# Kernel optimization log

Measured on AMD Instinct MI355X. Metric: run time of the kernel, lower is better.

## Reference

```python
import jax, jax.numpy as jnp
import numpy as np

B = 16384          # batch size
NUM_NEG = 4
N = 1 + NUM_NEG    # items per row (pos + negs)
D = 128            # embedding_dim
F = 4              # num_factors
FS = D // F        # factor_size = 32
TD = 384           # bert_text_dim
NU = 100000        # num_users
NI = 100000        # num_items
HID = 150          # text MLP hidden
M = 2              # num_modalities


def _linear_init(k, fan_out, fan_in):
    bound = 1.0 / np.sqrt(fan_in)
    return jax.random.uniform(k, (fan_out, fan_in), jnp.float32, -bound, bound)


def setup_inputs() -> dict:
    key = jax.random.key(0)
    ks = jax.random.split(key, 12)
    batch = jax.random.randint(ks[0], (B, 1 + N), 0, NU)          # col0=user, cols1..5=items
    text = jax.random.normal(ks[1], (B, N, TD), dtype=jnp.float32)
    user_table = jax.random.normal(ks[2], (NU, D), dtype=jnp.float32)
    item_table = jax.random.normal(ks[3], (NI, D), dtype=jnp.float32)
    w1 = _linear_init(ks[4], HID, TD)
    b1 = jax.random.uniform(ks[5], (HID,), jnp.float32, -1/np.sqrt(TD), 1/np.sqrt(TD))
    w2 = _linear_init(ks[6], D, HID)
    b2 = jax.random.uniform(ks[7], (D,), jnp.float32, -1/np.sqrt(HID), 1/np.sqrt(HID))
    # per-factor attention MLPs, stacked over the F factors (all same size here)
    aw1 = jax.random.uniform(ks[8], (F, M, 3 * FS), jnp.float32, -1/np.sqrt(3*FS), 1/np.sqrt(3*FS))
    ab1 = jax.random.uniform(ks[9], (F, M), jnp.float32, -1/np.sqrt(3*FS), 1/np.sqrt(3*FS))
    aw2 = jax.random.uniform(ks[10], (F, M, M), jnp.float32, -1/np.sqrt(M), 1/np.sqrt(M))
    return dict(batch=batch, text=text, user_table=user_table, item_table=item_table,
                w1=w1, b1=b1, w2=w2, b2=b2, aw1=aw1, ab1=ab1, aw2=aw2)


def _leaky_relu(x):
    return jnp.where(x > 0, x, 0.01 * x)


def reference(batch, text, user_table, item_table, w1, b1, w2, b2, aw1, ab1, aw2):
    # text MLP: Linear -> LeakyReLU -> Linear -> LeakyReLU
    te = _leaky_relu(_leaky_relu(text @ w1.T + b1) @ w2.T + b2)   # [B,N,D]

    users = batch[:, 0]
    items = batch[:, 1:]
    u = user_table[users]                                          # [B,D]
    ie = item_table[items]                                         # [B,N,D]

    # split into F factors of size FS (vectorized over factor dim)
    uf = jnp.broadcast_to(u[:, None, :], ie.shape).reshape(B, N, F, FS)
    itf = ie.reshape(B, N, F, FS)
    tf = te.reshape(B, N, F, FS)

    cat = jnp.concatenate([uf, itf, tf], axis=-1)                  # [B,N,F,3*FS]
    nrm = jnp.linalg.norm(cat, axis=-1, keepdims=True)
    cat = cat / jnp.maximum(nrm, 1e-12)                            # F.normalize(dim=-1)

    h = jnp.tanh(jnp.einsum('bnfk,fmk->bnfm', cat, aw1) + ab1)     # [B,N,F,M]
    logits = jnp.einsum('bnfm,fom->bnfo', h, aw2)                  # [B,N,F,M]
    # torch nn.Softmax() with dim=None on a 3D tensor -> softmax over dim 0 (batch)
    attn = jax.nn.softmax(logits, axis=0)

    r_ui = attn[..., 0] * jax.nn.softplus(jnp.sum(uf * itf, axis=-1))  # [B,N,F]
    r_ut = attn[..., 1] * jax.nn.softplus(jnp.sum(uf * tf, axis=-1))   # [B,N,F]
    ratings = jnp.sum(r_ui + r_ut, axis=-1)                        # [B,N], sum over factors
    return ratings
```

## Files before the change

kernel.cpp:

```cpp
#include <hip/hip_runtime.h>
#include <hip/hip_bf16.h>

#define TDIM 384
#define HID 150
#define DD 128
#define ROWS 81920
#define RT 64

typedef __attribute__((ext_vector_type(8))) short short8;
typedef __attribute__((ext_vector_type(4))) float f32x4;

#define SMEM_BYTES 35840

__device__ __forceinline__ float lrelu(float x) { return x > 0.f ? x : 0.01f * x; }
__device__ __forceinline__ float softplusf(float x) {
    return fmaxf(x, 0.f) + log1pf(expf(-fabsf(x)));
}

__device__ __forceinline__ short8 pack8(const float4 a, const float4 b) {
    union { short8 s; __hip_bfloat16 h[8]; } u;
    u.h[0] = __float2bfloat16(a.x); u.h[1] = __float2bfloat16(a.y);
    u.h[2] = __float2bfloat16(a.z); u.h[3] = __float2bfloat16(a.w);
    u.h[4] = __float2bfloat16(b.x); u.h[5] = __float2bfloat16(b.y);
    u.h[6] = __float2bfloat16(b.z); u.h[7] = __float2bfloat16(b.w);
    return u.s;
}

__global__ __launch_bounds__(256)
void prep_w(const float* __restrict__ w1, const float* __restrict__ w2,
            short8* __restrict__ w1f, short8* __restrict__ w2f)
{
    const int idx = blockIdx.x * 256 + threadIdx.x;
    union { short8 s; __hip_bfloat16 h[8]; } u;
    if (idx < 7680) {
        const int kt = idx / 640, c = idx % 640;
        const int col = c >> 2, q = c & 3;
        const int k = kt * 32 + q * 8;
#pragma unroll
        for (int j = 0; j < 8; ++j)
            u.h[j] = __float2bfloat16(col < HID ? w1[(size_t)col * TDIM + k + j] : 0.f);
        w1f[idx] = u.s;
    } else if (idx < 10240) {
        const int i2 = idx - 7680;
        const int kt = i2 / 512, c = i2 % 512;
        const int col = c >> 2, q = c & 3;
        const int k = kt * 32 + q * 8;
#pragma unroll
        for (int j = 0; j < 8; ++j)
            u.h[j] = __float2bfloat16((k + j) < HID ? w2[(size_t)col * HID + k + j] : 0.f);
        w2f[i2] = u.s;
    }
}

__global__ __launch_bounds__(256, 4)
void fused_main(const int* __restrict__ batch,
                const float* __restrict__ text,
                const float* __restrict__ user_table,
                const float* __restrict__ item_table,
                const short8* __restrict__ w1f,
                const float* __restrict__ b1,
                const short8* __restrict__ w2f,
                const float* __restrict__ b2,
                const float* __restrict__ aw1,
                const float* __restrict__ ab1,
                const float* __restrict__ aw2,
                float* __restrict__ expp,
                float* __restrict__ Sglob)
{
    __shared__ __align__(16) unsigned char smem[SMEM_BYTES];
    __shared__ float S_lds[40];
    __hip_bfloat16* Hs = (__hip_bfloat16*)(smem);
    float*          Ts = (float*)(smem);

    const int t    = threadIdx.x;
    const int r0   = blockIdx.x * RT;
    const int lane = t & 63;
    const int wv   = t >> 6;
    const int m16  = lane & 15;
    const int quad = lane >> 4;
    const int wr   = (wv & 1) * 32;
    const int wc   = (wv >> 1) * 80;
    const int wc2  = (wv >> 1) * 64;

    const int srow = t >> 2;
    const int sko  = (t & 3) * 8;
    const bool hasx = (t < 128);

    const int p3row = t >> 2;
    const int p3f   = t & 3;
    const int gr    = r0 + p3row;
    const int bb    = gr / 5;
    const int nn    = gr - bb * 5;
    const int uid   = batch[bb * 6];
    const int iid   = batch[bb * 6 + 1 + nn];

    if (t < 40) S_lds[t] = 0.f;

    f32x4 acc1[2][5];
#pragma unroll
    for (int i = 0; i < 2; ++i)
#pragma unroll
        for (int j = 0; j < 5; ++j) acc1[i][j] = (f32x4){0.f, 0.f, 0.f, 0.f};

    float4 pa0a, pa0b, pa1a, pa1b;
    short8 wr1a, wr1b, wr1c;

    const float* textp = &text[(size_t)(r0 + srow) * TDIM + sko];

    pa0a = *(const float4*)(textp);
    pa0b = *(const float4*)(textp + 4);
    wr1a = w1f[t];
    wr1b = w1f[t + 256];
    if (hasx) wr1c = w1f[t + 512];
    {
        __hip_bfloat16* As  = (__hip_bfloat16*)(smem);
        __hip_bfloat16* Ws1 = (__hip_bfloat16*)(smem + 10240);
        *(short8*)&As[srow * 40 + sko] = pack8(pa0a, pa0b);
        *(short8*)&Ws1[(t >> 2) * 40 + (t & 3) * 8] = wr1a;
        {
            const int c = t + 256;
            *(short8*)&Ws1[(c >> 2) * 40 + (c & 3) * 8] = wr1b;
        }
        if (hasx) {
            const int c = t + 512;
            *(short8*)&Ws1[(c >> 2) * 40 + (c & 3) * 8] = wr1c;
        }
    }
    pa1a = *(const float4*)(textp + 32);
    pa1b = *(const float4*)(textp + 36);
    __syncthreads();

#pragma unroll
    for (int kt = 0; kt < 12; ++kt) {
        const int p = kt & 1;
        if (kt < 10) {
            if (p == 0) {
                pa0a = *(const float4*)(textp + (kt + 2) * 32);
                pa0b = *(const float4*)(textp + (kt + 2) * 32 + 4);
            } else {
                pa1a = *(const float4*)(textp + (kt + 2) * 32);
                pa1b = *(const float4*)(textp + (kt + 2) * 32 + 4);
            }
        }
        if (kt < 11) {
            wr1a = w1f[(kt + 1) * 640 + t];
            wr1b = w1f[(kt + 1) * 640 + t + 256];
            if (hasx) wr1c = w1f[(kt + 1) * 640 + t + 512];
        }
        const __hip_bfloat16* As  = (const __hip_bfloat16*)(smem + p * 5120);
        const __hip_bfloat16* Ws1 = (const __hip_bfloat16*)(smem + 10240 + p * 12800);
        const short8 a0 = *(const short8*)&As[(wr + m16) * 40 + quad * 8];
        const short8 a1 = *(const short8*)&As[(wr + 16 + m16) * 40 + quad * 8];
#pragma unroll
        for (int tj = 0; tj < 5; ++tj) {
            const short8 b = *(const short8*)&Ws1[(wc + tj * 16 + m16) * 40 + quad * 8];
            acc1[0][tj] = __builtin_amdgcn_mfma_f32_16x16x32_bf16(a0, b, acc1[0][tj], 0, 0, 0);
            acc1[1][tj] = __builtin_amdgcn_mfma_f32_16x16x32_bf16(a1, b, acc1[1][tj], 0, 0, 0);
        }
        if (kt < 11) {
            __hip_bfloat16* Asn  = (__hip_bfloat16*)(smem + (p ^ 1) * 5120);
            __hip_bfloat16* Ws1n = (__hip_bfloat16*)(smem + 10240 + (p ^ 1) * 12800);
            *(short8*)&Asn[srow * 40 + sko] = (p == 0) ? pack8(pa1a, pa1b)
                                                       : pack8(pa0a, pa0b);
            *(short8*)&Ws1n[(t >> 2) * 40 + (t & 3) * 8] = wr1a;
            {
                const int c = t + 256;
                *(short8*)&Ws1n[(c >> 2) * 40 + (c & 3) * 8] = wr1b;
            }
            if (hasx) {
                const int c = t + 512;
                *(short8*)&Ws1n[(c >> 2) * 40 + (c & 3) * 8] = wr1c;
            }
        }
        __syncthreads();
    }

    short8 wr2a = w2f[t];
    short8 wr2b = w2f[t + 256];

#pragma unroll
    for (int tj = 0; tj < 5; ++tj) {
        const int col = wc + tj * 16 + m16;
        const float bv = (col < HID) ? b1[col] : 0.f;
#pragma unroll
        for (int ti = 0; ti < 2; ++ti) {
#pragma unroll
            for (int r = 0; r < 4; ++r) {
                const int row = wr + ti * 16 + quad * 4 + r;
                float v = lrelu(acc1[ti][tj][r] + bv);
                if (col >= HID) v = 0.f;
                Hs[row * 168 + col] = __float2bfloat16(v);
            }
        }
    }
    __syncthreads();

    f32x4 acc2[2][4];
#pragma unroll
    for (int i = 0; i < 2; ++i)
#pragma unroll
        for (int j = 0; j < 4; ++j) acc2[i][j] = (f32x4){0.f, 0.f, 0.f, 0.f};

#pragma unroll
    for (int kt = 0; kt < 5; ++kt) {
        {
            __hip_bfloat16* Ws2 = (__hip_bfloat16*)(smem + 21504);
            *(short8*)&Ws2[(t >> 2) * 40 + (t & 3) * 8] = wr2a;
            const int c = t + 256;
            *(short8*)&Ws2[(c >> 2) * 40 + (c & 3) * 8] = wr2b;
        }
        __syncthreads();
        if (kt < 4) {
            wr2a = w2f[(kt + 1) * 512 + t];
            wr2b = w2f[(kt + 1) * 512 + t + 256];
        }
        const int k0 = kt * 32;
        const __hip_bfloat16* Ws2 = (const __hip_bfloat16*)(smem + 21504);
        const short8 a0 = *(const short8*)&Hs[(wr + m16) * 168 + k0 + quad * 8];
        const short8 a1 = *(const short8*)&Hs[(wr + 16 + m16) * 168 + k0 + quad * 8];
#pragma unroll
        for (int tj = 0; tj < 4; ++tj) {
            const short8 b = *(const short8*)&Ws2[(wc2 + tj * 16 + m16) * 40 + quad * 8];
            acc2[0][tj] = __builtin_amdgcn_mfma_f32_16x16x32_bf16(a0, b, acc2[0][tj], 0, 0, 0);
            acc2[1][tj] = __builtin_amdgcn_mfma_f32_16x16x32_bf16(a1, b, acc2[1][tj], 0, 0, 0);
        }
        __syncthreads();
    }

    const float* up = user_table + (size_t)uid * DD + p3f * 32;
    const float* ip = item_table + (size_t)iid * DD + p3f * 32;
    float4 ur[8], er[8];
#pragma unroll
    for (int q = 0; q < 8; ++q) {
        ur[q] = *(const float4*)(up + q * 4);
        er[q] = *(const float4*)(ip + q * 4);
    }

#pragma unroll
    for (int tj = 0; tj < 4; ++tj) {
        const int col = wc2 + tj * 16 + m16;
        const float bv = b2[col];
#pragma unroll
        for (int ti = 0; ti < 2; ++ti) {
#pragma unroll
            for (int r = 0; r < 4; ++r) {
                const int row = wr + ti * 16 + quad * 4 + r;
                Ts[row * 132 + col] = lrelu(acc2[ti][tj][r] + bv);
            }
        }
    }
    __syncthreads();

    {
        const float* tp  = Ts + p3row * 132 + p3f * 32;
        const float* a1p = aw1 + p3f * 2 * 96;

        float ss = 0.f, z0 = 0.f, z1 = 0.f, sui = 0.f, sut = 0.f;
#pragma unroll
        for (int q = 0; q < 8; ++q) {
            const float4 u4 = ur[q];
            const float4 e4 = er[q];
            const float4 t4 = *(const float4*)(tp + q * 4);
            const float4 a00 = *(const float4*)(a1p + q * 4);
            const float4 a01 = *(const float4*)(a1p + 32 + q * 4);
            const float4 a02 = *(const float4*)(a1p + 64 + q * 4);
            const float4 a10 = *(const float4*)(a1p + 96 + q * 4);
            const float4 a11 = *(const float4*)(a1p + 128 + q * 4);
            const float4 a12 = *(const float4*)(a1p + 160 + q * 4);
            const float uu[4] = {u4.x, u4.y, u4.z, u4.w};
            const float ee[4] = {e4.x, e4.y, e4.z, e4.w};
            const float tt[4] = {t4.x, t4.y, t4.z, t4.w};
            const float w00[4] = {a00.x, a00.y, a00.z, a00.w};
            const float w01[4] = {a01.x, a01.y, a01.z, a01.w};
            const float w02[4] = {a02.x, a02.y, a02.z, a02.w};
            const float w10[4] = {a10.x, a10.y, a10.z, a10.w};
            const float w11[4] = {a11.x, a11.y, a11.z, a11.w};
            const float w12[4] = {a12.x, a12.y, a12.z, a12.w};
#pragma unroll
            for (int c = 0; c < 4; ++c) {
                const float u = uu[c], e = ee[c], x = tt[c];
                ss  = fmaf(u, u, ss); ss = fmaf(e, e, ss); ss = fmaf(x, x, ss);
                z0  = fmaf(u, w00[c], z0);
                z0  = fmaf(e, w01[c], z0);
                z0  = fmaf(x, w02[c], z0);
                z1  = fmaf(u, w10[c], z1);
                z1  = fmaf(e, w11[c], z1);
                z1  = fmaf(x, w12[c], z1);
                sui = fmaf(u, e, sui);
                sut = fmaf(u, x, sut);
            }
        }
        const float inv = 1.f / fmaxf(sqrtf(ss), 1e-12f);
        const float h0 = tanhf(fmaf(z0, inv, ab1[p3f * 2 + 0]));
        const float h1 = tanhf(fmaf(z1, inv, ab1[p3f * 2 + 1]));
        const float l0 = fmaf(h0, aw2[p3f * 4 + 0], h1 * aw2[p3f * 4 + 1]);
        const float l1 = fmaf(h0, aw2[p3f * 4 + 2], h1 * aw2[p3f * 4 + 3]);
        const float e0 = expf(l0), e1 = expf(l1);
        const float pui = softplusf(sui), put = softplusf(sut);
        *(float4*)&expp[((size_t)gr * 4 + p3f) * 4] = make_float4(e0, e1, pui, put);
        atomicAdd(&S_lds[nn * 8 + p3f * 2 + 0], e0);
        atomicAdd(&S_lds[nn * 8 + p3f * 2 + 1], e1);
    }
    __syncthreads();
    if (t < 40) atomicAdd(&Sglob[t * 32], S_lds[t]);
}

__global__ void finalize(const float* __restrict__ expp,
                         const float* __restrict__ Sglob,
                         float* __restrict__ out)
{
    const int gr = blockIdx.x * 256 + threadIdx.x;
    if (gr >= ROWS) return;
    const int b = gr / 5;
    const int n = gr - b * 5;
    float r = 0.f;
#pragma unroll
    for (int f = 0; f < 4; ++f) {
        const float4 v = *(const float4*)&expp[((size_t)gr * 4 + f) * 4];
        const float S0 = Sglob[(n * 8 + f * 2 + 0) * 32];
        const float S1 = Sglob[(n * 8 + f * 2 + 1) * 32];
        r += v.x / S0 * v.z + v.y / S1 * v.w;
    }
    out[gr] = r;
}

extern "C" void kernel_launch(void* const* d_in, const int* in_sizes, int n_in,
                              void* d_out, int out_size, void* d_ws, size_t ws_size,
                              hipStream_t stream)
{
    (void)in_sizes; (void)n_in; (void)out_size; (void)ws_size;
    const int*   batch      = (const int*)d_in[0];
    const float* text       = (const float*)d_in[1];
    const float* user_table = (const float*)d_in[2];
    const float* item_table = (const float*)d_in[3];
    const float* w1         = (const float*)d_in[4];
    const float* b1         = (const float*)d_in[5];
    const float* w2         = (const float*)d_in[6];
    const float* b2         = (const float*)d_in[7];
    const float* aw1        = (const float*)d_in[8];
    const float* ab1        = (const float*)d_in[9];
    const float* aw2        = (const float*)d_in[10];
    float* out = (float*)d_out;

    char* ws = (char*)d_ws;
    short8* w1f   = (short8*)ws;
    short8* w2f   = (short8*)(ws + 122880);
    float*  expp  = (float*)(ws + 163840);
    float*  Sglob = (float*)(ws + 163840 + (size_t)ROWS * 16 * 4);

    hipMemsetAsync(Sglob, 0, 40 * 32 * sizeof(float), stream);
    prep_w<<<40, 256, 0, stream>>>(w1, w2, w1f, w2f);
    fused_main<<<ROWS / RT, 256, 0, stream>>>(batch, text, user_table, item_table,
                                              w1f, b1, w2f, b2, aw1, ab1, aw2,
                                              expp, Sglob);
    finalize<<<(ROWS + 255) / 256, 256, 0, stream>>>(expp, Sglob, out);
}
```

Measured before the change: 345.3 us.

## Load GEMM operands directly into MFMA registers, drop LDS staging and LDS atomics

The first GEMM now loads text rows and pre-swizzled W1 fragments straight from global memory into per-lane registers in MFMA operand layout. This removes the double-buffered LDS tiles and the per-k-step barriers. The second GEMM likewise reads W2 fragments directly from global instead of staging them in LDS. The per-block softmax partial sums move from LDS atomics to a plain store followed by a strided serial reduction by 40 threads. The cost is more redundant global and L2 traffic for weight fragments, since each wave re-reads them instead of sharing them through LDS.

Result: no change. 352.2 us (+2.0%).

```diff
diff --git a/kernel.cpp b/kernel.cpp
--- a/kernel.cpp
+++ b/kernel.cpp
@@ -10,7 +10,7 @@
 typedef __attribute__((ext_vector_type(8))) short short8;
 typedef __attribute__((ext_vector_type(4))) float f32x4;
 
-#define SMEM_BYTES 35840
+#define SMEM_BYTES 33792
 
 __device__ __forceinline__ float lrelu(float x) { return x > 0.f ? x : 0.01f * x; }
 __device__ __forceinline__ float softplusf(float x) {
@@ -68,7 +68,7 @@
                 float* __restrict__ Sglob)
 {
     __shared__ __align__(16) unsigned char smem[SMEM_BYTES];
-    __shared__ float S_lds[40];
+    __shared__ __align__(8) float red[512];
     __hip_bfloat16* Hs = (__hip_bfloat16*)(smem);
     float*          Ts = (float*)(smem);
 
@@ -82,10 +82,6 @@
     const int wc   = (wv >> 1) * 80;
     const int wc2  = (wv >> 1) * 64;
 
-    const int srow = t >> 2;
-    const int sko  = (t & 3) * 8;
-    const bool hasx = (t < 128);
-
     const int p3row = t >> 2;
     const int p3f   = t & 3;
     const int gr    = r0 + p3row;
@@ -94,7 +90,10 @@
     const int uid   = batch[bb * 6];
     const int iid   = batch[bb * 6 + 1 + nn];
 
-    if (t < 40) S_lds[t] = 0.f;
+    const float* ta  = text + (size_t)(r0 + wr + m16) * TDIM;
+    const float* tb  = ta + 16 * TDIM;
+    const int    ko0 = quad * 8;
+    const int w1base = (wc + m16) * 4 + quad;
 
     f32x4 acc1[2][5];
 #pragma unroll
@@ -102,81 +101,37 @@
 #pragma unroll
         for (int j = 0; j < 5; ++j) acc1[i][j] = (f32x4){0.f, 0.f, 0.f, 0.f};
 
-    float4 pa0a, pa0b, pa1a, pa1b;
-    short8 wr1a, wr1b, wr1c;
-
-    const float* textp = &text[(size_t)(r0 + srow) * TDIM + sko];
-
-    pa0a = *(const float4*)(textp);
-    pa0b = *(const float4*)(textp + 4);
-    wr1a = w1f[t];
-    wr1b = w1f[t + 256];
-    if (hasx) wr1c = w1f[t + 512];
-    {
-        __hip_bfloat16* As  = (__hip_bfloat16*)(smem);
-        __hip_bfloat16* Ws1 = (__hip_bfloat16*)(smem + 10240);
-        *(short8*)&As[srow * 40 + sko] = pack8(pa0a, pa0b);
-        *(short8*)&Ws1[(t >> 2) * 40 + (t & 3) * 8] = wr1a;
-        {
-            const int c = t + 256;
-            *(short8*)&Ws1[(c >> 2) * 40 + (c & 3) * 8] = wr1b;
-        }
-        if (hasx) {
-            const int c = t + 512;
-            *(short8*)&Ws1[(c >> 2) * 40 + (c & 3) * 8] = wr1c;
-        }
-    }
-    pa1a = *(const float4*)(textp + 32);
-    pa1b = *(const float4*)(textp + 36);
-    __syncthreads();
+    float4 pA[2][4];
+#pragma unroll
+    for (int k = 0; k < 2; ++k) {
+        pA[k][0] = *(const float4*)(ta + k * 32 + ko0);
+        pA[k][1] = *(const float4*)(ta + k * 32 + ko0 + 4);
+        pA[k][2] = *(const float4*)(tb + k * 32 + ko0);
+        pA[k][3] = *(const float4*)(tb + k * 32 + ko0 + 4);
+    }
 
 #pragma unroll
     for (int kt = 0; kt < 12; ++kt) {
         const int p = kt & 1;
+        short8 bw[5];
+#pragma unroll
+        for (int tj = 0; tj < 5; ++tj)
+            bw[tj] = w1f[kt * 640 + w1base + tj * 64];
+        const short8 a0 = pack8(pA[p][0], pA[p][1]);
+        const short8 a1 = pack8(pA[p][2], pA[p][3]);
         if (kt < 10) {
-            if (p == 0) {
-                pa0a = *(const float4*)(textp + (kt + 2) * 32);
-                pa0b = *(const float4*)(textp + (kt + 2) * 32 + 4);
-            } else {
-                pa1a = *(const float4*)(textp + (kt + 2) * 32);
-                pa1b = *(const float4*)(textp + (kt + 2) * 32 + 4);
-            }
-        }
-        if (kt < 11) {
-            wr1a = w1f[(kt + 1) * 640 + t];
-            wr1b = w1f[(kt + 1) * 640 + t + 256];
-            if (hasx) wr1c = w1f[(kt + 1) * 640 + t + 512];
-        }
-        const __hip_bfloat16* As  = (const __hip_bfloat16*)(smem + p * 5120);
-        const __hip_bfloat16* Ws1 = (const __hip_bfloat16*)(smem + 10240 + p * 12800);
-        const short8 a0 = *(const short8*)&As[(wr + m16) * 40 + quad * 8];
-        const short8 a1 = *(const short8*)&As[(wr + 16 + m16) * 40 + quad * 8];
+            const int ko = (kt + 2) * 32 + ko0;
+            pA[p][0] = *(const float4*)(ta + ko);
+            pA[p][1] = *(const float4*)(ta + ko + 4);
+            pA[p][2] = *(const float4*)(tb + ko);
+            pA[p][3] = *(const float4*)(tb + ko + 4);
+        }
 #pragma unroll
         for (int tj = 0; tj < 5; ++tj) {
-            const short8 b = *(const short8*)&Ws1[(wc + tj * 16 + m16) * 40 + quad * 8];
-            acc1[0][tj] = __builtin_amdgcn_mfma_f32_16x16x32_bf16(a0, b, acc1[0][tj], 0, 0, 0);
-            acc1[1][tj] = __builtin_amdgcn_mfma_f32_16x16x32_bf16(a1, b, acc1[1][tj], 0, 0, 0);
-        }
-        if (kt < 11) {
-            __hip_bfloat16* Asn  = (__hip_bfloat16*)(smem + (p ^ 1) * 5120);
-            __hip_bfloat16* Ws1n = (__hip_bfloat16*)(smem + 10240 + (p ^ 1) * 12800);
-            *(short8*)&Asn[srow * 40 + sko] = (p == 0) ? pack8(pa1a, pa1b)
-                                                       : pack8(pa0a, pa0b);
-            *(short8*)&Ws1n[(t >> 2) * 40 + (t & 3) * 8] = wr1a;
-            {
-                const int c = t + 256;
-                *(short8*)&Ws1n[(c >> 2) * 40 + (c & 3) * 8] = wr1b;
-            }
-            if (hasx) {
-                const int c = t + 512;
-                *(short8*)&Ws1n[(c >> 2) * 40 + (c & 3) * 8] = wr1c;
-            }
-        }
-        __syncthreads();
-    }
-
-    short8 wr2a = w2f[t];
-    short8 wr2b = w2f[t + 256];
+            acc1[0][tj] = __builtin_amdgcn_mfma_f32_16x16x32_bf16(a0, bw[tj], acc1[0][tj], 0, 0, 0);
+            acc1[1][tj] = __builtin_amdgcn_mfma_f32_16x16x32_bf16(a1, bw[tj], acc1[1][tj], 0, 0, 0);
+        }
+    }
 
 #pragma unroll
     for (int tj = 0; tj < 5; ++tj) {
@@ -201,40 +156,25 @@
 #pragma unroll
         for (int j = 0; j < 4; ++j) acc2[i][j] = (f32x4){0.f, 0.f, 0.f, 0.f};
 
+    const __hip_bfloat16* h0p = Hs + (wr + m16) * 168 + ko0;
+    const __hip_bfloat16* h1p = h0p + 16 * 168;
+    const int w2base = (wc2 + m16) * 4 + quad;
+
 #pragma unroll
     for (int kt = 0; kt < 5; ++kt) {
-        {
-            __hip_bfloat16* Ws2 = (__hip_bfloat16*)(smem + 21504);
-            *(short8*)&Ws2[(t >> 2) * 40 + (t & 3) * 8] = wr2a;
-            const int c = t + 256;
-            *(short8*)&Ws2[(c >> 2) * 40 + (c & 3) * 8] = wr2b;
-        }
-        __syncthreads();
-        if (kt < 4) {
-            wr2a = w2f[(kt + 1) * 512 + t];
-            wr2b = w2f[(kt + 1) * 512 + t + 256];
-        }
-        const int k0 = kt * 32;
-        const __hip_bfloat16* Ws2 = (const __hip_bfloat16*)(smem + 21504);
-        const short8 a0 = *(const short8*)&Hs[(wr + m16) * 168 + k0 + quad * 8];
-        const short8 a1 = *(const short8*)&Hs[(wr + 16 + m16) * 168 + k0 + quad * 8];
+        short8 bw[4];
+#pragma unroll
+        for (int tj = 0; tj < 4; ++tj)
+            bw[tj] = w2f[kt * 512 + w2base + tj * 64];
+        const short8 a0 = *(const short8*)(h0p + kt * 32);
+        const short8 a1 = *(const short8*)(h1p + kt * 32);
 #pragma unroll
         for (int tj = 0; tj < 4; ++tj) {
-            const short8 b = *(const short8*)&Ws2[(wc2 + tj * 16 + m16) * 40 + quad * 8];
-            acc2[0][tj] = __builtin_amdgcn_mfma_f32_16x16x32_bf16(a0, b, acc2[0][tj], 0, 0, 0);
-            acc2[1][tj] = __builtin_amdgcn_mfma_f32_16x16x32_bf16(a1, b, acc2[1][tj], 0, 0, 0);
-        }
-        __syncthreads();
-    }
-
-    const float* up = user_table + (size_t)uid * DD + p3f * 32;
-    const float* ip = item_table + (size_t)iid * DD + p3f * 32;
-    float4 ur[8], er[8];
-#pragma unroll
-    for (int q = 0; q < 8; ++q) {
-        ur[q] = *(const float4*)(up + q * 4);
-        er[q] = *(const float4*)(ip + q * 4);
-    }
+            acc2[0][tj] = __builtin_amdgcn_mfma_f32_16x16x32_bf16(a0, bw[tj], acc2[0][tj], 0, 0, 0);
+            acc2[1][tj] = __builtin_amdgcn_mfma_f32_16x16x32_bf16(a1, bw[tj], acc2[1][tj], 0, 0, 0);
+        }
+    }
+    __syncthreads();
 
 #pragma unroll
     for (int tj = 0; tj < 4; ++tj) {
@@ -248,6 +188,15 @@
                 Ts[row * 132 + col] = lrelu(acc2[ti][tj][r] + bv);
             }
         }
+    }
+
+    const float* up = user_table + (size_t)uid * DD + p3f * 32;
+    const float* ip = item_table + (size_t)iid * DD + p3f * 32;
+    float4 ur[8], er[8];
+#pragma unroll
+    for (int q = 0; q < 8; ++q) {
+        ur[q] = *(const float4*)(up + q * 4);
+        er[q] = *(const float4*)(ip + q * 4);
     }
     __syncthreads();
 
@@ -298,11 +247,19 @@
         const float e0 = expf(l0), e1 = expf(l1);
         const float pui = softplusf(sui), put = softplusf(sut);
         *(float4*)&expp[((size_t)gr * 4 + p3f) * 4] = make_float4(e0, e1, pui, put);
-        atomicAdd(&S_lds[nn * 8 + p3f * 2 + 0], e0);
-        atomicAdd(&S_lds[nn * 8 + p3f * 2 + 1], e1);
+        *(float2*)&red[p3row * 8 + p3f * 2] = make_float2(e0, e1);
     }
     __syncthreads();
-    if (t < 40) atomicAdd(&Sglob[t * 32], S_lds[t]);
+
+    if (t < 40) {
+        const int j   = t & 7;
+        const int nn0 = t >> 3;
+        int r = nn0 - (r0 % 5);
+        if (r < 0) r += 5;
+        float s = 0.f;
+        for (; r < RT; r += 5) s += red[r * 8 + j];
+        atomicAdd(&Sglob[t * 32], s);
+    }
 }
 
 __global__ void finalize(const float* __restrict__ expp,
```
